# Performance work log

Hardware: AMD Instinct MI355X
Metric: run time of the kernel (lower is better)

Reference implementation:

```python
import jax, jax.numpy as jnp
import numpy as np


def setup_inputs() -> dict:
    key = jax.random.key(0)
    ks = jax.random.split(key, 6)
    B, N, d = 4096, 32768, 512
    return {
        "X_src": jax.random.normal(ks[0], (B, d), dtype=jnp.float32),
        "X_trans": jax.random.normal(ks[1], (B, d), dtype=jnp.float32),
        "Y_tgt": jax.random.normal(ks[2], (B, d), dtype=jnp.float32),
        "Z_src": jax.random.normal(ks[3], (N, d), dtype=jnp.float32),
        "Z_trans": jax.random.normal(ks[4], (N, d), dtype=jnp.float32),
        "Z_tgt": jax.random.normal(ks[5], (N, d), dtype=jnp.float32),
        "knn": 10,
    }


def _getknn(sc, k):
    # torch: topk(10) indices[:, :k], gather, sum  ==  sum of top-k values per row
    vals, _ = jax.lax.top_k(sc, k)  # [rows, k]
    return vals.sum() / k


def reference(X_src, X_trans, Y_tgt, Z_src, Z_trans, Z_tgt, knn):
    B = X_src.shape[0]
    f = 2.0 * (X_trans * Y_tgt).sum()
    # sc0: [B, N] similarity of translated src words vs target vocab
    fk0 = _getknn(X_trans @ Z_tgt.T, knn)
    # Z_trans.mm(Y_tgt.t()).t() == Y_tgt @ Z_trans.T : [B, N]
    fk1 = _getknn(Y_tgt @ Z_trans.T, knn)
    f = f - fk0 - fk1
    return -f / B
```

## Files before the change

### kernel.cpp

```cpp
#include <hip/hip_runtime.h>
#include <hip/hip_bf16.h>
#include <float.h>
#include <cstdint>


#define B_ROWS 4096
#define N_COLS 32768
#define D_K    512
#define NCHUNK (N_COLS / 128)

typedef __bf16 bf16x8 __attribute__((ext_vector_type(8)));
typedef float  f32x16 __attribute__((ext_vector_type(16)));
typedef unsigned short u16x2 __attribute__((ext_vector_type(2)));

__device__ __forceinline__ unsigned short f2bf(float f) {
    unsigned int u = __float_as_uint(f);
    u += 0x7FFFu + ((u >> 16) & 1u);
    return (unsigned short)(u >> 16);
}
__device__ __forceinline__ unsigned f2sort32(float f) {
    unsigned u = __float_as_uint(f);
    u += 0x7FFFu + ((u >> 16) & 1u);
    return u ^ (0x80000000u | (unsigned)((int)u >> 31));
}
__device__ __forceinline__ float sort2f(unsigned int y) {
    unsigned int x = (y & 0x8000u) ? (y ^ 0x8000u) : (~y & 0xFFFFu);
    return __uint_as_float(x << 16);
}
__device__ __forceinline__ unsigned umax(unsigned a, unsigned b) { return a > b ? a : b; }
__device__ __forceinline__ unsigned umin(unsigned a, unsigned b) { return a < b ? a : b; }

__device__ __forceinline__ void gload_lds16(const void* g, void* l) {
    __builtin_amdgcn_global_load_lds(
        (const __attribute__((address_space(1))) unsigned int*)(uintptr_t)g,
        (__attribute__((address_space(3))) unsigned int*)(uintptr_t)l,
        16, 0, 0);
}

__global__ void zero_scalars(float* sc) {
    if (threadIdx.x < 3) sc[threadIdx.x] = 0.0f;
}

__global__ void prep_kernel(const float4* __restrict__ X,
                            const float4* __restrict__ Y,
                            const float4* __restrict__ Zt,
                            const float4* __restrict__ Ztr,
                            ushort4* __restrict__ A0, ushort4* __restrict__ A1,
                            ushort4* __restrict__ B0, ushort4* __restrict__ B1,
                            float* __restrict__ dotacc) {
    const int z = blockIdx.y;
    int i = blockIdx.x * 256 + threadIdx.x;
    const int stride = gridDim.x * 256;
    if (z == 0) {
        float s = 0.0f;
        for (; i < B_ROWS * D_K / 4; i += stride) {
            float4 x = X[i], y = Y[i];
            ushort4 u; u.x = f2bf(x.x); u.y = f2bf(x.y);
            u.z = f2bf(x.z); u.w = f2bf(x.w);
            A0[i] = u;
            s += x.x * y.x + x.y * y.y + x.z * y.z + x.w * y.w;
        }
        for (int o = 32; o > 0; o >>= 1) s += __shfl_down(s, o);
        __shared__ float wsum[4];
        int lane = threadIdx.x & 63, w = threadIdx.x >> 6;
        if (lane == 0) wsum[w] = s;
        __syncthreads();
        if (threadIdx.x == 0)
            atomicAdd(dotacc, wsum[0] + wsum[1] + wsum[2] + wsum[3]);
    } else {
        const float4* src = (z == 1) ? Y : (z == 2) ? Zt : Ztr;
        ushort4* dst = (z == 1) ? A1 : (z == 2) ? B0 : B1;
        int n4 = (z == 1) ? (B_ROWS * D_K / 4) : (N_COLS * D_K / 4);
        for (; i < n4; i += stride) {
            float4 f = src[i];
            ushort4 u; u.x = f2bf(f.x); u.y = f2bf(f.y);
            u.z = f2bf(f.z); u.w = f2bf(f.w);
            dst[i] = u;
        }
    }
}

#define BARRIER()  asm volatile("s_barrier" ::: "memory")
#define VMCNT(N)   asm volatile("s_waitcnt vmcnt(" #N ")" ::: "memory")
#define LGKM0()    asm volatile("s_waitcnt lgkmcnt(0)" ::: "memory")

#define STAGE(T) do { \
    gload_lds16(gA + (T) * 32,      smem + ((T) & 3) * 16384 + (w * 2 + 0) * 512); \
    gload_lds16(gA + (T) * 32 + 16, smem + ((T) & 3) * 16384 + (w * 2 + 1) * 512); \
    gload_lds16(gB + (T) * 32,      smem + ((T) & 3) * 16384 + 8192 + (w * 2 + 0) * 512); \
    gload_lds16(gB + (T) * 32 + 16, smem + ((T) & 3) * 16384 + 8192 + (w * 2 + 1) * 512); \
} while (0)

#define LOADH(AF, BF, SLOT, KK) { \
    _Pragma("unroll") for (int rb = 0; rb < 4; ++rb) \
        AF[rb] = *(const bf16x8*)(smem + (SLOT) * 16384 + ((wm * 4 + rb) * 2 + (KK)) * 512 + lane8); \
    _Pragma("unroll") for (int cb = 0; cb < 2; ++cb) \
        BF[cb] = *(const bf16x8*)(smem + (SLOT) * 16384 + 8192 + ((wn * 2 + cb) * 2 + (KK)) * 512 + lane8); \
}

#define MFMAH(AF, BF) { \
    _Pragma("unroll") for (int rb = 0; rb < 4; ++rb) { \
    _Pragma("unroll") for (int cb = 0; cb < 2; ++cb) { \
        acc[rb][cb] = __builtin_amdgcn_mfma_f32_32x32x16_bf16( \
            BF[cb], AF[rb], acc[rb][cb], 0, 0, 0); } } }

#define KSTEP(J) do { \
    LOADH(afn, bfn, (J) & 3, 1); \
    MFMAH(afc, bfc); \
    if ((J) < 15) LOADH(afc, bfc, ((J) + 1) & 3, 0); \
    MFMAH(afn, bfn); \
    if ((J) < 12)       { LGKM0(); VMCNT(4); BARRIER(); STAGE((J) + 4); } \
    else if ((J) == 12) { VMCNT(4); BARRIER(); } \
    else if ((J) == 13) { VMCNT(0); BARRIER(); } \
} while (0)

#define CSWAP(a, b) { unsigned _hi = umax(a, b), _lo = umin(a, b); a = _hi; b = _lo; }
#define SORT4() { CSWAP(m0, m1); CSWAP(m2, m3); CSWAP(m0, m2); CSWAP(m1, m3); CSWAP(m1, m2); }
#define INS(V) { u16x2 _hi; \
    _hi = __builtin_elementwise_max(t0, V); V = __builtin_elementwise_min(t0, V); t0 = _hi; \
    _hi = __builtin_elementwise_max(t1, V); V = __builtin_elementwise_min(t1, V); t1 = _hi; \
    _hi = __builtin_elementwise_max(t2, V); V = __builtin_elementwise_min(t2, V); t2 = _hi; \
    _hi = __builtin_elementwise_max(t3, V); V = __builtin_elementwise_min(t3, V); t3 = _hi; }

__global__ __launch_bounds__(512, 2)
void gemm_topk_kernel(const unsigned short* __restrict__ A0g,
                      const unsigned short* __restrict__ A1g,
                      const unsigned short* __restrict__ B0g,
                      const unsigned short* __restrict__ B1g,
                      uint2* __restrict__ P0, uint2* __restrict__ P1) {
    const unsigned short* A  = blockIdx.y ? A1g : A0g;
    const unsigned short* Bm = blockIdx.y ? B1g : B0g;
    uint2* P2 = blockIdx.y ? P1 : P0;

    __shared__ __align__(128) unsigned short smem[4 * 16384];

    const int tid   = threadIdx.x;
    const int lane  = tid & 63;
    const int w     = tid >> 6;
    const int wm    = w >> 2;
    const int wn    = w & 3;
    const int rlane = lane & 31;
    const int hi    = lane >> 5;
    const int lane8 = lane * 8;

    const int b      = blockIdx.x;
    const int xcd    = b & 7;
    const int ii     = b >> 3;
    const int cw     = ii & 7;
    const int rowblk = (ii >> 3) & 15;
    const int cg     = ii >> 7;
    const int bn     = xcd * 16 + cg * 8 + cw;
    const int row0   = rowblk * 256;
    const int col0   = bn * 256;

    const unsigned short* gA = A  + (size_t)(row0 + w * 32 + rlane) * D_K + hi * 8;
    const unsigned short* gB = Bm + (size_t)(col0 + w * 32 + rlane) * D_K + hi * 8;

    f32x16 acc[4][2];
    #pragma unroll
    for (int rb = 0; rb < 4; ++rb)
        #pragma unroll
        for (int cb = 0; cb < 2; ++cb)
            #pragma unroll
            for (int e = 0; e < 16; ++e)
                acc[rb][cb][e] = 0.0f;

    bf16x8 afc[4], afn[4], bfc[2], bfn[2];

    STAGE(0);
    STAGE(1);
    STAGE(2);
    STAGE(3);
    VMCNT(8);
    BARRIER();
    LOADH(afc, bfc, 0, 0)

    KSTEP(0);  KSTEP(1);  KSTEP(2);  KSTEP(3);
    KSTEP(4);  KSTEP(5);  KSTEP(6);  KSTEP(7);
    KSTEP(8);  KSTEP(9);  KSTEP(10); KSTEP(11);
    KSTEP(12); KSTEP(13); KSTEP(14); KSTEP(15);

    const int chunk = bn * 2 + (wn >> 1);
    const int half  = wn & 1;
    #pragma unroll
    for (int rb = 0; rb < 4; ++rb) {
        u16x2 t0 = {0, 0}, t1 = {0, 0}, t2 = {0, 0}, t3 = {0, 0};
        #pragma unroll
        for (int cb = 0; cb < 2; ++cb) {
            #pragma unroll
            for (int p = 0; p < 8; ++p) {
                unsigned sa = f2sort32(acc[rb][cb][2 * p]);
                unsigned sb = f2sort32(acc[rb][cb][2 * p + 1]);
                unsigned pk = (sa >> 16) | (sb & 0xFFFF0000u);
                u16x2 v = *(u16x2*)&pk;
                INS(v);
            }
        }
        unsigned m0 = umax((unsigned)t0.x, (unsigned)t3.y);
        unsigned m1 = umax((unsigned)t1.x, (unsigned)t2.y);
        unsigned m2 = umax((unsigned)t2.x, (unsigned)t1.y);
        unsigned m3 = umax((unsigned)t3.x, (unsigned)t0.y);
        SORT4();
        {
            unsigned pa = m0 | (m1 << 16);
            unsigned pb = m2 | (m3 << 16);
            unsigned qa = (unsigned)__shfl_xor((int)pa, 32);
            unsigned qb = (unsigned)__shfl_xor((int)pb, 32);
            unsigned ra = (qa >> 16) | (qa << 16);
            unsigned rb2 = (qb >> 16) | (qb << 16);
            u16x2 n0 = __builtin_elementwise_max(*(u16x2*)&pa, *(u16x2*)&rb2);
            u16x2 n1 = __builtin_elementwise_max(*(u16x2*)&pb, *(u16x2*)&ra);
            m0 = n0.x; m1 = n0.y; m2 = n1.x; m3 = n1.y;
            SORT4();
        }
        if (hi == 0) {
            int row_g = row0 + wm * 128 + rb * 32 + rlane;
            P2[((size_t)row_g * NCHUNK + chunk) * 2 + half] =
                make_uint2(m0 | (m1 << 16), m2 | (m3 << 16));
        }
    }
}

__global__ __launch_bounds__(256, 4)
void merge_topk_kernel(const unsigned int* __restrict__ P0,
                       const unsigned int* __restrict__ P1,
                       float* __restrict__ sc) {
    const int g    = blockIdx.y;
    const int lane = threadIdx.x & 63;
    const int w    = threadIdx.x >> 6;
    const int row  = blockIdx.x * 4 + w;
    const unsigned int* Rp = (g ? P1 : P0) + (size_t)row * (NCHUNK * 4);

    u16x2 t[10];
    #pragma unroll
    for (int i = 0; i < 10; ++i) t[i] = (u16x2){0, 0};
    #pragma unroll 4
    for (int it = 0; it < 16; ++it) {
        unsigned int raw = Rp[lane + 64 * it];
        u16x2 v = *(u16x2*)&raw;
        #pragma unroll
        for (int i = 0; i < 10; ++i) {
            u16x2 hi = __builtin_elementwise_max(t[i], v);
            v = __builtin_elementwise_min(t[i], v);
            t[i] = hi;
        }
    }
    unsigned int wreg[10];
    #pragma unroll
    for (int i = 0; i < 10; ++i) {
        unsigned int mv = umax((unsigned int)t[i].x,
                               (unsigned int)t[9 - i].y);
        wreg[i] = (mv << 16) | ((unsigned int)lane << 4) | (unsigned int)i;
    }
    float sum10 = 0.0f;
    #pragma unroll
    for (int iter = 0; iter < 10; ++iter) {
        unsigned int mx = wreg[0];
        #pragma unroll
        for (int s = 1; s < 10; ++s) mx = umax(mx, wreg[s]);
        #pragma unroll
        for (int o = 32; o > 0; o >>= 1)
            mx = umax(mx, (unsigned int)__shfl_xor((int)mx, o));
        sum10 += sort2f(mx >> 16);
        #pragma unroll
        for (int s = 0; s < 10; ++s)
            if (wreg[s] == mx) wreg[s] = 0u;
    }
    if (lane == 0) atomicAdd(sc + 1 + g, sum10);
}

__global__ void finalize_kernel(const float* __restrict__ sc,
                                float* __restrict__ out) {
    if (threadIdx.x == 0) {
        float f = (sc[1] * 0.1f + sc[2] * 0.1f - 2.0f * sc[0]) * (1.0f / 4096.0f);
        out[0] = f;
    }
}

extern "C" void kernel_launch(void* const* d_in, const int* in_sizes, int n_in,
                              void* d_out, int out_size, void* d_ws, size_t ws_size,
                              hipStream_t stream) {
    const float* X_trans = (const float*)d_in[1];
    const float* Y_tgt   = (const float*)d_in[2];
    const float* Z_trans = (const float*)d_in[4];
    const float* Z_tgt   = (const float*)d_in[5];

    char* ws = (char*)d_ws;
    float* sc = (float*)ws;
    unsigned short* A0 = (unsigned short*)(ws + 256);
    unsigned short* A1 = A0 + (size_t)B_ROWS * D_K;
    unsigned short* B0 = A1 + (size_t)B_ROWS * D_K;
    unsigned short* B1 = B0 + (size_t)N_COLS * D_K;
    uint2* P0 = (uint2*)(B1 + (size_t)N_COLS * D_K);
    uint2* P1 = P0 + (size_t)B_ROWS * NCHUNK * 2;

    zero_scalars<<<1, 64, 0, stream>>>(sc);

    dim3 pgrid(2048, 4);
    prep_kernel<<<pgrid, 256, 0, stream>>>(
        (const float4*)X_trans, (const float4*)Y_tgt,
        (const float4*)Z_tgt, (const float4*)Z_trans,
        (ushort4*)A0, (ushort4*)A1, (ushort4*)B0, (ushort4*)B1, sc + 0);

    dim3 ggrid(2048, 2);
    gemm_topk_kernel<<<ggrid, 512, 0, stream>>>(A0, A1, B0, B1, P0, P1);

    dim3 mgrid(B_ROWS / 4, 2);
    merge_topk_kernel<<<mgrid, 256, 0, stream>>>(
        (const unsigned int*)P0, (const unsigned int*)P1, sc);

    finalize_kernel<<<1, 64, 0, stream>>>(sc, (float*)d_out);
}
```

Before: 692.4 us.

## Restructure GEMM K-loop into ping-pong half-steps with split A/B staging and setprio

```diff
diff --git a/kernel.cpp b/kernel.cpp
--- a/kernel.cpp
+++ b/kernel.cpp
@@ -84,11 +84,13 @@
 #define VMCNT(N)   asm volatile("s_waitcnt vmcnt(" #N ")" ::: "memory")
 #define LGKM0()    asm volatile("s_waitcnt lgkmcnt(0)" ::: "memory")
 
-#define STAGE(T) do { \
+#define STAGE_A(T) do { if ((T) <= 15) { \
     gload_lds16(gA + (T) * 32,      smem + ((T) & 3) * 16384 + (w * 2 + 0) * 512); \
-    gload_lds16(gA + (T) * 32 + 16, smem + ((T) & 3) * 16384 + (w * 2 + 1) * 512); \
+    gload_lds16(gA + (T) * 32 + 16, smem + ((T) & 3) * 16384 + (w * 2 + 1) * 512); } \
+} while (0)
+#define STAGE_B(T) do { if ((T) <= 15) { \
     gload_lds16(gB + (T) * 32,      smem + ((T) & 3) * 16384 + 8192 + (w * 2 + 0) * 512); \
-    gload_lds16(gB + (T) * 32 + 16, smem + ((T) & 3) * 16384 + 8192 + (w * 2 + 1) * 512); \
+    gload_lds16(gB + (T) * 32 + 16, smem + ((T) & 3) * 16384 + 8192 + (w * 2 + 1) * 512); } \
 } while (0)
 
 #define LOADH(AF, BF, SLOT, KK) { \
@@ -105,13 +107,27 @@
             BF[cb], AF[rb], acc[rb][cb], 0, 0, 0); } } }
 
 #define KSTEP(J) do { \
+     \
+    LOADH(afc, bfc, (J) & 3, 0); \
+    STAGE_A((J) + 3); \
+    BARRIER(); \
+    LGKM0(); \
+    __builtin_amdgcn_s_setprio(1); \
+    MFMAH(afc, bfc); \
+    __builtin_amdgcn_s_setprio(0); \
+    BARRIER(); \
+     \
     LOADH(afn, bfn, (J) & 3, 1); \
-    MFMAH(afc, bfc); \
-    if ((J) < 15) LOADH(afc, bfc, ((J) + 1) & 3, 0); \
+    STAGE_B((J) + 3); \
+    BARRIER(); \
+    LGKM0(); \
+    __builtin_amdgcn_s_setprio(1); \
     MFMAH(afn, bfn); \
-    if ((J) < 12)       { LGKM0(); VMCNT(4); BARRIER(); STAGE((J) + 4); } \
-    else if ((J) == 12) { VMCNT(4); BARRIER(); } \
-    else if ((J) == 13) { VMCNT(0); BARRIER(); } \
+    __builtin_amdgcn_s_setprio(0); \
+    if ((J) <= 12)      { VMCNT(8); } \
+    else if ((J) == 13) { VMCNT(4); } \
+    else if ((J) == 14) { VMCNT(0); } \
+    BARRIER(); \
 } while (0)
 
 #define CSWAP(a, b) { unsigned _hi = umax(a, b), _lo = umin(a, b); a = _hi; b = _lo; }
@@ -167,13 +183,11 @@
 
     bf16x8 afc[4], afn[4], bfc[2], bfn[2];
 
-    STAGE(0);
-    STAGE(1);
-    STAGE(2);
-    STAGE(3);
+    STAGE_A(0); STAGE_B(0);
+    STAGE_A(1); STAGE_B(1);
+    STAGE_A(2); STAGE_B(2);
     VMCNT(8);
     BARRIER();
-    LOADH(afc, bfc, 0, 0)
 
     KSTEP(0);  KSTEP(1);  KSTEP(2);  KSTEP(3);
     KSTEP(4);  KSTEP(5);  KSTEP(6);  KSTEP(7);
```

New measurement: 692.0 us. About the same (-0.1%).

## Shrink GEMM tiles to 128x128 with 4 waves and triple-buffered LDS

Applied to the files above, without the earlier changes.

```diff
diff --git a/kernel.cpp b/kernel.cpp
--- a/kernel.cpp
+++ b/kernel.cpp
@@ -85,33 +85,33 @@
 #define LGKM0()    asm volatile("s_waitcnt lgkmcnt(0)" ::: "memory")
 
 #define STAGE(T) do { \
-    gload_lds16(gA + (T) * 32,      smem + ((T) & 3) * 16384 + (w * 2 + 0) * 512); \
-    gload_lds16(gA + (T) * 32 + 16, smem + ((T) & 3) * 16384 + (w * 2 + 1) * 512); \
-    gload_lds16(gB + (T) * 32,      smem + ((T) & 3) * 16384 + 8192 + (w * 2 + 0) * 512); \
-    gload_lds16(gB + (T) * 32 + 16, smem + ((T) & 3) * 16384 + 8192 + (w * 2 + 1) * 512); \
+    gload_lds16(gA + (T) * 32,      smem + ((T) % 3) * 8192 + (w * 2 + 0) * 512); \
+    gload_lds16(gA + (T) * 32 + 16, smem + ((T) % 3) * 8192 + (w * 2 + 1) * 512); \
+    gload_lds16(gB + (T) * 32,      smem + ((T) % 3) * 8192 + 4096 + (w * 2 + 0) * 512); \
+    gload_lds16(gB + (T) * 32 + 16, smem + ((T) % 3) * 8192 + 4096 + (w * 2 + 1) * 512); \
 } while (0)
 
 #define LOADH(AF, BF, SLOT, KK) { \
-    _Pragma("unroll") for (int rb = 0; rb < 4; ++rb) \
-        AF[rb] = *(const bf16x8*)(smem + (SLOT) * 16384 + ((wm * 4 + rb) * 2 + (KK)) * 512 + lane8); \
+    _Pragma("unroll") for (int rb = 0; rb < 2; ++rb) \
+        AF[rb] = *(const bf16x8*)(smem + (SLOT) * 8192 + ((wm * 2 + rb) * 2 + (KK)) * 512 + lane8); \
     _Pragma("unroll") for (int cb = 0; cb < 2; ++cb) \
-        BF[cb] = *(const bf16x8*)(smem + (SLOT) * 16384 + 8192 + ((wn * 2 + cb) * 2 + (KK)) * 512 + lane8); \
+        BF[cb] = *(const bf16x8*)(smem + (SLOT) * 8192 + 4096 + ((wn * 2 + cb) * 2 + (KK)) * 512 + lane8); \
 }
 
 #define MFMAH(AF, BF) { \
-    _Pragma("unroll") for (int rb = 0; rb < 4; ++rb) { \
+    _Pragma("unroll") for (int rb = 0; rb < 2; ++rb) { \
     _Pragma("unroll") for (int cb = 0; cb < 2; ++cb) { \
         acc[rb][cb] = __builtin_amdgcn_mfma_f32_32x32x16_bf16( \
             BF[cb], AF[rb], acc[rb][cb], 0, 0, 0); } } }
 
 #define KSTEP(J) do { \
-    LOADH(afn, bfn, (J) & 3, 1); \
-    MFMAH(afc, bfc); \
-    if ((J) < 15) LOADH(afc, bfc, ((J) + 1) & 3, 0); \
-    MFMAH(afn, bfn); \
-    if ((J) < 12)       { LGKM0(); VMCNT(4); BARRIER(); STAGE((J) + 4); } \
-    else if ((J) == 12) { VMCNT(4); BARRIER(); } \
-    else if ((J) == 13) { VMCNT(0); BARRIER(); } \
+    LOADH(af0, bf0, (J) % 3, 0); \
+    LOADH(af1, bf1, (J) % 3, 1); \
+    if ((J) <= 13) STAGE((J) + 2); \
+    MFMAH(af0, bf0); \
+    MFMAH(af1, bf1); \
+    if ((J) <= 13)      { LGKM0(); VMCNT(4); BARRIER(); } \
+    else if ((J) == 14) { LGKM0(); VMCNT(0); BARRIER(); } \
 } while (0)
 
 #define CSWAP(a, b) { unsigned _hi = umax(a, b), _lo = umin(a, b); a = _hi; b = _lo; }
@@ -122,7 +122,7 @@
     _hi = __builtin_elementwise_max(t2, V); V = __builtin_elementwise_min(t2, V); t2 = _hi; \
     _hi = __builtin_elementwise_max(t3, V); V = __builtin_elementwise_min(t3, V); t3 = _hi; }
 
-__global__ __launch_bounds__(512, 2)
+__global__ __launch_bounds__(256, 3)
 void gemm_topk_kernel(const unsigned short* __restrict__ A0g,
                       const unsigned short* __restrict__ A1g,
                       const unsigned short* __restrict__ B0g,
@@ -132,13 +132,13 @@
     const unsigned short* Bm = blockIdx.y ? B1g : B0g;
     uint2* P2 = blockIdx.y ? P1 : P0;
 
-    __shared__ __align__(128) unsigned short smem[4 * 16384];
+    __shared__ __align__(128) unsigned short smem[3 * 8192];
 
     const int tid   = threadIdx.x;
     const int lane  = tid & 63;
     const int w     = tid >> 6;
-    const int wm    = w >> 2;
-    const int wn    = w & 3;
+    const int wm    = w >> 1;
+    const int wn    = w & 1;
     const int rlane = lane & 31;
     const int hi    = lane >> 5;
     const int lane8 = lane * 8;
@@ -147,43 +147,40 @@
     const int xcd    = b & 7;
     const int ii     = b >> 3;
     const int cw     = ii & 7;
-    const int rowblk = (ii >> 3) & 15;
-    const int cg     = ii >> 7;
-    const int bn     = xcd * 16 + cg * 8 + cw;
-    const int row0   = rowblk * 256;
-    const int col0   = bn * 256;
+    const int rowblk = (ii >> 3) & 31;
+    const int cg     = ii >> 8;
+    const int bn     = xcd * 32 + cg * 8 + cw;
+    const int row0   = rowblk * 128;
+    const int col0   = bn * 128;
 
     const unsigned short* gA = A  + (size_t)(row0 + w * 32 + rlane) * D_K + hi * 8;
     const unsigned short* gB = Bm + (size_t)(col0 + w * 32 + rlane) * D_K + hi * 8;
 
-    f32x16 acc[4][2];
-    #pragma unroll
-    for (int rb = 0; rb < 4; ++rb)
+    f32x16 acc[2][2];
+    #pragma unroll
+    for (int rb = 0; rb < 2; ++rb)
         #pragma unroll
         for (int cb = 0; cb < 2; ++cb)
             #pragma unroll
             for (int e = 0; e < 16; ++e)
                 acc[rb][cb][e] = 0.0f;
 
-    bf16x8 afc[4], afn[4], bfc[2], bfn[2];
+    bf16x8 af0[2], af1[2], bf0[2], bf1[2];
 
     STAGE(0);
     STAGE(1);
-    STAGE(2);
-    STAGE(3);
-    VMCNT(8);
+    VMCNT(4);
     BARRIER();
-    LOADH(afc, bfc, 0, 0)
 
     KSTEP(0);  KSTEP(1);  KSTEP(2);  KSTEP(3);
     KSTEP(4);  KSTEP(5);  KSTEP(6);  KSTEP(7);
     KSTEP(8);  KSTEP(9);  KSTEP(10); KSTEP(11);
     KSTEP(12); KSTEP(13); KSTEP(14); KSTEP(15);
 
-    const int chunk = bn * 2 + (wn >> 1);
-    const int half  = wn & 1;
-    #pragma unroll
-    for (int rb = 0; rb < 4; ++rb) {
+    const int chunk = bn;
+    const int half  = wn;
+    #pragma unroll
+    for (int rb = 0; rb < 2; ++rb) {
         u16x2 t0 = {0, 0}, t1 = {0, 0}, t2 = {0, 0}, t3 = {0, 0};
         #pragma unroll
         for (int cb = 0; cb < 2; ++cb) {
@@ -214,7 +211,7 @@
             SORT4();
         }
         if (hi == 0) {
-            int row_g = row0 + wm * 128 + rb * 32 + rlane;
+            int row_g = row0 + wm * 64 + rb * 32 + rlane;
             P2[((size_t)row_g * NCHUNK + chunk) * 2 + half] =
                 make_uint2(m0 | (m1 << 16), m2 | (m3 << 16));
         }
@@ -302,8 +299,8 @@
         (const float4*)Z_tgt, (const float4*)Z_trans,
         (ushort4*)A0, (ushort4*)A1, (ushort4*)B0, (ushort4*)B1, sc + 0);
 
-    dim3 ggrid(2048, 2);
-    gemm_topk_kernel<<<ggrid, 512, 0, stream>>>(A0, A1, B0, B1, P0, P1);
+    dim3 ggrid(8192, 2);
+    gemm_topk_kernel<<<ggrid, 256, 0, stream>>>(A0, A1, B0, B1, P0, P1);
 
     dim3 mgrid(B_ROWS / 4, 2);
     merge_topk_kernel<<<mgrid, 256, 0, stream>>>(
```

After: 808.2 us. +16.7%, slower.
